# Kernel optimization log

Measured on AMD Instinct MI355X. Metric: run time of the kernel, lower is better.

## Reference

```python
import jax, jax.numpy as jnp
import numpy as np

B, T, IN, H, STEPS = 32768, 11, 2, 64, 80


def gru_cell(x, h, W_ih, W_hh, b_ih, b_hh):
    # PyTorch GRU cell: gates ordered (r, z, n)
    gi = x @ W_ih.T + b_ih            # [B, 3H]
    gh = h @ W_hh.T + b_hh            # [B, 3H]
    gi_r, gi_z, gi_n = jnp.split(gi, 3, axis=-1)
    gh_r, gh_z, gh_n = jnp.split(gh, 3, axis=-1)
    r = jax.nn.sigmoid(gi_r + gh_r)
    z = jax.nn.sigmoid(gi_z + gh_z)
    n = jnp.tanh(gi_n + r * gh_n)
    return (1.0 - z) * n + z * h


def setup_inputs() -> dict:
    key = jax.random.key(0)
    ks = jax.random.split(key, 20)
    s = 1.0 / np.sqrt(H)
    u = lambda k, shape: jax.random.uniform(k, shape, jnp.float32, -s, s)
    inp = {"x": jax.random.normal(ks[0], (B, T, IN), jnp.float32)}
    i = 1
    for pfx, in0 in (("e", IN), ("d", IN)):
        for l, d_in in ((0, in0), (1, H)):
            inp[f"{pfx}W_ih{l}"] = u(ks[i], (3 * H, d_in)); i += 1
            inp[f"{pfx}W_hh{l}"] = u(ks[i], (3 * H, H)); i += 1
            inp[f"{pfx}b_ih{l}"] = u(ks[i], (3 * H,)); i += 1
            inp[f"{pfx}b_hh{l}"] = u(ks[i], (3 * H,)); i += 1
    inp["fc_W"] = u(ks[17], (2, H))
    inp["fc_b"] = u(ks[18], (2,))
    return inp


def reference(x, eW_ih0, eW_hh0, eb_ih0, eb_hh0, eW_ih1, eW_hh1, eb_ih1, eb_hh1,
              dW_ih0, dW_hh0, db_ih0, db_hh0, dW_ih1, dW_hh1, db_ih1, db_hh1,
              fc_W, fc_b):
    b = x.shape[0]
    h0 = jnp.zeros((b, H), x.dtype)
    h1 = jnp.zeros((b, H), x.dtype)

    # ---- encoder: 2-layer GRU over time (dropout inactive in eval) ----
    def enc_step(carry, xt):
        c0, c1 = carry
        c0 = gru_cell(xt, c0, eW_ih0, eW_hh0, eb_ih0, eb_hh0)
        c1 = gru_cell(c0, c1, eW_ih1, eW_hh1, eb_ih1, eb_hh1)
        return (c0, c1), None

    (h0, h1), _ = jax.lax.scan(enc_step, (h0, h1), jnp.swapaxes(x, 0, 1))

    def dec_step(carry, _):
        inp, c0, c1 = carry
        c0 = gru_cell(inp, c0, dW_ih0, dW_hh0, db_ih0, db_hh0)
        c1 = gru_cell(c0, c1, dW_ih1, dW_hh1, db_ih1, db_hh1)
        pred = c1 @ fc_W.T + fc_b     # [B, 2]
        return (pred, c0, c1), pred

    init = (x[:, -1, :], h0, h1)
    _, preds = jax.lax.scan(dec_step, init, None, length=STEPS)  # [80, B, 2]
    return jnp.swapaxes(preds, 0, 1)  # [B, 80, 2]
```

## Files before the change

### kernel.cpp

```cpp
#include <hip/hip_runtime.h>
#include <cstddef>

#define T_SEQ 11
#define STEPS 80

typedef _Float16 f16;
typedef _Float16 f16x4 __attribute__((ext_vector_type(4)));
typedef _Float16 f16x8 __attribute__((ext_vector_type(8)));
typedef float    f32x4 __attribute__((ext_vector_type(4)));

#define SRC (-1.44269504f)
#define SNC ( 2.88539008f)

__device__ __forceinline__ f32x4 mfma16(f16x8 a, f16x8 b, f32x4 c) {
    return __builtin_amdgcn_mfma_f32_16x16x32_f16(a, b, c, 0, 0, 0);
}
__device__ __forceinline__ float exp2r(float x) { return __builtin_amdgcn_exp2f(x); }

__device__ __forceinline__ f16x8 wfrag(const float* __restrict__ W, int row, int k0, float sc) {
    f16x8 r;
    #pragma unroll
    for (int i = 0; i < 8; ++i) r[i] = (f16)(sc * W[row * 64 + k0 + i]);
    return r;
}
__device__ __forceinline__ f16x8 cfrag(const float* __restrict__ Wih0,
                                       const float* __restrict__ fcW, int row, int k0, float sc) {
    f16x8 r;
    #pragma unroll
    for (int i = 0; i < 8; ++i)
        r[i] = (f16)(sc * (Wih0[row * 2] * fcW[k0 + i] + Wih0[row * 2 + 1] * fcW[64 + k0 + i]));
    return r;
}

struct WSet {
    f16x8 xR[2], xZ[2], xN[2];
    f16x8 hR[2], hZ[2], hN[2];
    f32x4 bR, bZ, bNi, bNh;
};

__device__ __forceinline__ void load_h_side(WSet& W,
    const float* __restrict__ Whh, const float* __restrict__ bih,
    const float* __restrict__ bhh, int jA, int j4, int quad)
{
    #pragma unroll
    for (int ks = 0; ks < 2; ++ks) {
        const int k0 = ks * 32 + quad * 8;
        W.hR[ks] = wfrag(Whh, jA,       k0, SRC);
        W.hZ[ks] = wfrag(Whh, jA + 64,  k0, SRC);
        W.hN[ks] = wfrag(Whh, jA + 128, k0, SNC);
    }
    #pragma unroll
    for (int rg = 0; rg < 4; ++rg) {
        W.bR[rg]  = SRC * (bih[j4 + rg] + bhh[j4 + rg]);
        W.bZ[rg]  = SRC * (bih[64 + j4 + rg] + bhh[64 + j4 + rg]);
        W.bNi[rg] = SNC * bih[128 + j4 + rg];
        W.bNh[rg] = SNC * bhh[128 + j4 + rg];
    }
}
__device__ __forceinline__ void load_x_side(WSet& W, const float* __restrict__ Wx,
                                            int jA, int quad)
{
    #pragma unroll
    for (int ks = 0; ks < 2; ++ks) {
        const int k0 = ks * 32 + quad * 8;
        W.xR[ks] = wfrag(Wx, jA,       k0, SRC);
        W.xZ[ks] = wfrag(Wx, jA + 64,  k0, SRC);
        W.xN[ks] = wfrag(Wx, jA + 128, k0, SNC);
    }
}

template<bool XM>
__device__ __forceinline__ void cell(const WSet& W,
    const f16* __restrict__ Xs, const f16* __restrict__ Hs, f16* __restrict__ Dst,
    f16x4 (&ho)[4],
    const f32x4* __restrict__ xw, const float2* __restrict__ xv,
    int ro0, int ro1, int wo)
{
    #pragma unroll
    for (int mt = 0; mt < 4; ++mt) {
        const int mo = mt * 1024;
        f16x8 hb0 = *(const f16x8*)(Hs + ro0 + mo);
        f16x8 hb1 = *(const f16x8*)(Hs + ro1 + mo);
        f32x4 aR  = mfma16(W.hR[0], hb0, W.bR);
        f32x4 aZ  = mfma16(W.hZ[0], hb0, W.bZ);
        f32x4 aNh = mfma16(W.hN[0], hb0, W.bNh);
        aR  = mfma16(W.hR[1], hb1, aR);
        aZ  = mfma16(W.hZ[1], hb1, aZ);
        aNh = mfma16(W.hN[1], hb1, aNh);
        f32x4 aNi;
        if constexpr (XM) {
            f16x8 xb0 = *(const f16x8*)(Xs + ro0 + mo);
            f16x8 xb1 = *(const f16x8*)(Xs + ro1 + mo);
            aR  = mfma16(W.xR[0], xb0, aR);    aR  = mfma16(W.xR[1], xb1, aR);
            aZ  = mfma16(W.xZ[0], xb0, aZ);    aZ  = mfma16(W.xZ[1], xb1, aZ);
            aNi = mfma16(W.xN[0], xb0, W.bNi); aNi = mfma16(W.xN[1], xb1, aNi);
        } else {
            const float x0 = xv[mt].x, x1 = xv[mt].y;
            aR  += x0 * xw[0] + x1 * xw[1];
            aZ  += x0 * xw[2] + x1 * xw[3];
            aNi  = W.bNi + x0 * xw[4] + x1 * xw[5];
        }
        f16x4 o;
        #pragma unroll
        for (int i = 0; i < 4; ++i) {
            const float r = __builtin_amdgcn_rcpf(1.f + exp2r(aR[i]));
            const float z = __builtin_amdgcn_rcpf(1.f + exp2r(aZ[i]));
            const float n = 1.f - 2.f * __builtin_amdgcn_rcpf(1.f + exp2r(aNi[i] + r * aNh[i]));
            const float h = n + z * ((float)ho[mt][i] - n);
            o[i] = (f16)h;
        }
        ho[mt] = o;
        *(f16x4*)(Dst + wo + mo) = o;
    }
}

__global__ __launch_bounds__(256, 2)
void gru_traj_mfma8(
    const float* __restrict__ x,
    const float* __restrict__ eWih0, const float* __restrict__ eWhh0,
    const float* __restrict__ ebih0, const float* __restrict__ ebhh0,
    const float* __restrict__ eWih1, const float* __restrict__ eWhh1,
    const float* __restrict__ ebih1, const float* __restrict__ ebhh1,
    const float* __restrict__ dWih0, const float* __restrict__ dWhh0,
    const float* __restrict__ dbih0, const float* __restrict__ dbhh0,
    const float* __restrict__ dWih1, const float* __restrict__ dWhh1,
    const float* __restrict__ dbih1, const float* __restrict__ dbhh1,
    const float* __restrict__ fcW,  const float* __restrict__ fcb,
    float* __restrict__ out)
{
    __shared__ f16 hbuf[4][64 * 64];
    __shared__ float2 xe[T_SEQ * 64];

    const int tid  = threadIdx.x;
    const int lane = tid & 63;
    const int w    = __builtin_amdgcn_readfirstlane(tid >> 6);
    const int quad = lane >> 4;
    const int col  = lane & 15;
    const int r0   = blockIdx.x * 64;

    {
        const float2* x2 = (const float2*)x;
        for (int i = tid; i < 64 * T_SEQ; i += 256) {
            const int row = i / T_SEQ, t = i - row * T_SEQ;
            xe[t * 64 + row] = x2[(size_t)r0 * T_SEQ + i];
        }
    }
    for (int i = tid; i < 64 * 64; i += 256) { hbuf[0][i] = (f16)0.f; hbuf[2][i] = (f16)0.f; }

    const int c7  = col & 7;
    const int ro0 = col * 64 + ((quad ^ c7) << 3);
    const int ro1 = col * 64 + (((4 + quad) ^ c7) << 3);
    const int wo  = col * 64 + ((((w << 1) | (quad >> 1)) ^ c7) << 3) + ((quad & 1) << 2);

    const int jA = w * 16 + col;
    const int j4 = w * 16 + quad * 4;

    f16x4 ho0[4], ho1[4];
    #pragma unroll
    for (int mt = 0; mt < 4; ++mt) {
        #pragma unroll
        for (int i = 0; i < 4; ++i) { ho0[mt][i] = (f16)0.f; ho1[mt][i] = (f16)0.f; }
    }

    WSet W0, W1;
    load_h_side(W0, eWhh0, ebih0, ebhh0, jA, j4, quad);
    load_h_side(W1, eWhh1, ebih1, ebhh1, jA, j4, quad);
    load_x_side(W1, eWih1, jA, quad);
    {
        f32x4 xw[6];
        #pragma unroll
        for (int rg = 0; rg < 4; ++rg) {
            xw[0][rg] = SRC * eWih0[(j4 + rg) * 2];        xw[1][rg] = SRC * eWih0[(j4 + rg) * 2 + 1];
            xw[2][rg] = SRC * eWih0[(64 + j4 + rg) * 2];   xw[3][rg] = SRC * eWih0[(64 + j4 + rg) * 2 + 1];
            xw[4][rg] = SNC * eWih0[(128 + j4 + rg) * 2];  xw[5][rg] = SNC * eWih0[(128 + j4 + rg) * 2 + 1];
        }
        __syncthreads();

        #pragma unroll 1
        for (int t = 0; t < T_SEQ - 1; t += 2) {
            float2 xv[4];
            #pragma unroll
            for (int mt = 0; mt < 4; ++mt) xv[mt] = xe[t * 64 + mt * 16 + col];
            cell<false>(W0, hbuf[0], hbuf[0], hbuf[1], ho0, xw, xv, ro0, ro1, wo);
            __syncthreads();
            cell<true >(W1, hbuf[1], hbuf[2], hbuf[3], ho1, nullptr, nullptr, ro0, ro1, wo);
            #pragma unroll
            for (int mt = 0; mt < 4; ++mt) xv[mt] = xe[(t + 1) * 64 + mt * 16 + col];
            cell<false>(W0, hbuf[1], hbuf[1], hbuf[0], ho0, xw, xv, ro0, ro1, wo);
            __syncthreads();
            cell<true >(W1, hbuf[0], hbuf[3], hbuf[2], ho1, nullptr, nullptr, ro0, ro1, wo);
        }
        {
            float2 xv[4];
            #pragma unroll
            for (int mt = 0; mt < 4; ++mt) xv[mt] = xe[10 * 64 + mt * 16 + col];
            cell<false>(W0, hbuf[0], hbuf[0], hbuf[1], ho0, xw, xv, ro0, ro1, wo);
            __syncthreads();
            cell<true >(W1, hbuf[1], hbuf[2], hbuf[3], ho1, nullptr, nullptr, ro0, ro1, wo);
        }
    }

    load_h_side(W0, dWhh0, dbih0, dbhh0, jA, j4, quad);
    #pragma unroll
    for (int ks = 0; ks < 2; ++ks) {
        const int k0 = ks * 32 + quad * 8;
        W0.xR[ks] = cfrag(dWih0, fcW, jA,       k0, SRC);
        W0.xZ[ks] = cfrag(dWih0, fcW, jA + 64,  k0, SRC);
        W0.xN[ks] = cfrag(dWih0, fcW, jA + 128, k0, SNC);
    }
    #pragma unroll
    for (int rg = 0; rg < 4; ++rg) {
        const int j = j4 + rg;
        W0.bR[rg]  += SRC * (dWih0[j * 2] * fcb[0]         + dWih0[j * 2 + 1] * fcb[1]);
        W0.bZ[rg]  += SRC * (dWih0[(64 + j) * 2] * fcb[0]  + dWih0[(64 + j) * 2 + 1] * fcb[1]);
        W0.bNi[rg] += SNC * (dWih0[(128 + j) * 2] * fcb[0] + dWih0[(128 + j) * 2 + 1] * fcb[1]);
    }
    load_h_side(W1, dWhh1, dbih1, dbhh1, jA, j4, quad);
    load_x_side(W1, dWih1, jA, quad);
    f16x8 fcf[2];
    #pragma unroll
    for (int ks = 0; ks < 2; ++ks) {
        #pragma unroll
        for (int i = 0; i < 8; ++i) fcf[ks][i] = (f16)0.f;
        if (col < 2) fcf[ks] = wfrag(fcW, col, ks * 32 + quad * 8, 1.0f);
    }
    f32x4 pb;
    #pragma unroll
    for (int rg = 0; rg < 4; ++rg) pb[rg] = (quad == 0 && rg < 2) ? fcb[rg] : 0.f;

    float* __restrict__ op = out + (size_t)(r0 + w * 16 + col) * (STEPS * 2);

    {
        f32x4 xw[6];
        #pragma unroll
        for (int rg = 0; rg < 4; ++rg) {
            xw[0][rg] = SRC * dWih0[(j4 + rg) * 2];        xw[1][rg] = SRC * dWih0[(j4 + rg) * 2 + 1];
            xw[2][rg] = SRC * dWih0[(64 + j4 + rg) * 2];   xw[3][rg] = SRC * dWih0[(64 + j4 + rg) * 2 + 1];
            xw[4][rg] = SNC * dWih0[(128 + j4 + rg) * 2];  xw[5][rg] = SNC * dWih0[(128 + j4 + rg) * 2 + 1];
        }
        float2 xv0[4];
        #pragma unroll
        for (int mt = 0; mt < 4; ++mt) xv0[mt] = xe[10 * 64 + mt * 16 + col];
        cell<false>(W0, hbuf[1], hbuf[1], hbuf[0], ho0, xw, xv0, ro0, ro1, wo);
        __syncthreads();
        cell<true >(W1, hbuf[0], hbuf[3], hbuf[2], ho1, nullptr, nullptr, ro0, ro1, wo);
        __syncthreads();
        f16x8 hb0 = *(const f16x8*)(hbuf[2] + ro0 + w * 1024);
        f16x8 hb1 = *(const f16x8*)(hbuf[2] + ro1 + w * 1024);
        f32x4 p = mfma16(fcf[0], hb0, pb);
        p = mfma16(fcf[1], hb1, p);
        if (quad == 0) *(float2*)op = make_float2(p[0], p[1]);
        op += 2;
    }

    #pragma unroll 1
    for (int sp = 0; sp < 39; ++sp) {
        cell<true>(W0, hbuf[2], hbuf[0], hbuf[1], ho0, nullptr, nullptr, ro0, ro1, wo);
        __syncthreads();
        cell<true>(W1, hbuf[1], hbuf[2], hbuf[3], ho1, nullptr, nullptr, ro0, ro1, wo);
        __syncthreads();
        {
            f16x8 hb0 = *(const f16x8*)(hbuf[3] + ro0 + w * 1024);
            f16x8 hb1 = *(const f16x8*)(hbuf[3] + ro1 + w * 1024);
            f32x4 p = mfma16(fcf[0], hb0, pb);
            p = mfma16(fcf[1], hb1, p);
            if (quad == 0) *(float2*)op = make_float2(p[0], p[1]);
            op += 2;
        }
        cell<true>(W0, hbuf[3], hbuf[1], hbuf[0], ho0, nullptr, nullptr, ro0, ro1, wo);
        __syncthreads();
        cell<true>(W1, hbuf[0], hbuf[3], hbuf[2], ho1, nullptr, nullptr, ro0, ro1, wo);
        __syncthreads();
        {
            f16x8 hb0 = *(const f16x8*)(hbuf[2] + ro0 + w * 1024);
            f16x8 hb1 = *(const f16x8*)(hbuf[2] + ro1 + w * 1024);
            f32x4 p = mfma16(fcf[0], hb0, pb);
            p = mfma16(fcf[1], hb1, p);
            if (quad == 0) *(float2*)op = make_float2(p[0], p[1]);
            op += 2;
        }
    }
    {
        cell<true>(W0, hbuf[2], hbuf[0], hbuf[1], ho0, nullptr, nullptr, ro0, ro1, wo);
        __syncthreads();
        cell<true>(W1, hbuf[1], hbuf[2], hbuf[3], ho1, nullptr, nullptr, ro0, ro1, wo);
        __syncthreads();
        f16x8 hb0 = *(const f16x8*)(hbuf[3] + ro0 + w * 1024);
        f16x8 hb1 = *(const f16x8*)(hbuf[3] + ro1 + w * 1024);
        f32x4 p = mfma16(fcf[0], hb0, pb);
        p = mfma16(fcf[1], hb1, p);
        if (quad == 0) *(float2*)op = make_float2(p[0], p[1]);
    }
}

extern "C" void kernel_launch(void* const* d_in, const int* in_sizes, int n_in,
                              void* d_out, int out_size, void* d_ws, size_t ws_size,
                              hipStream_t stream) {
    (void)n_in; (void)out_size; (void)d_ws; (void)ws_size;

    const float* x     = (const float*)d_in[0];
    const float* eWih0 = (const float*)d_in[1];
    const float* eWhh0 = (const float*)d_in[2];
    const float* ebih0 = (const float*)d_in[3];
    const float* ebhh0 = (const float*)d_in[4];
    const float* eWih1 = (const float*)d_in[5];
    const float* eWhh1 = (const float*)d_in[6];
    const float* ebih1 = (const float*)d_in[7];
    const float* ebhh1 = (const float*)d_in[8];
    const float* dWih0 = (const float*)d_in[9];
    const float* dWhh0 = (const float*)d_in[10];
    const float* dbih0 = (const float*)d_in[11];
    const float* dbhh0 = (const float*)d_in[12];
    const float* dWih1 = (const float*)d_in[13];
    const float* dWhh1 = (const float*)d_in[14];
    const float* dbih1 = (const float*)d_in[15];
    const float* dbhh1 = (const float*)d_in[16];
    const float* fcW   = (const float*)d_in[17];
    const float* fcb   = (const float*)d_in[18];
    float* out = (float*)d_out;

    const int b = in_sizes[0] / (T_SEQ * 2);
    dim3 grid(b / 64), block(256);
    hipLaunchKernelGGL(gru_traj_mfma8, grid, block, 0, stream,
        x, eWih0, eWhh0, ebih0, ebhh0, eWih1, eWhh1, ebih1, ebhh1,
        dWih0, dWhh0, dbih0, dbhh0, dWih1, dWhh1, dbih1, dbhh1,
        fcW, fcb, out);
}
```

Measured before the change: 450.4 us.

## Halve rows per block to 32 and raise occupancy to four blocks per CU

Each block now processes 32 batch rows instead of 64, which halves the per-thread hidden-state registers, the per-step MFMA tiles and the shared buffers. The grid doubles and launch bounds ask for four resident blocks per CU instead of two. More resident blocks can hide barrier and MFMA latency in the serial recurrence. In exchange, the per-thread weight fragments are duplicated across twice as many blocks, and only two of the four waves now do the output projection.

Result: slower. 1.621 ms (+259.9%).

```diff
diff --git a/kernel.cpp b/kernel.cpp
--- a/kernel.cpp
+++ b/kernel.cpp
@@ -72,12 +72,12 @@
 template<bool XM>
 __device__ __forceinline__ void cell(const WSet& W,
     const f16* __restrict__ Xs, const f16* __restrict__ Hs, f16* __restrict__ Dst,
-    f16x4 (&ho)[4],
+    f16x4 (&ho)[2],
     const f32x4* __restrict__ xw, const float2* __restrict__ xv,
     int ro0, int ro1, int wo)
 {
     #pragma unroll
-    for (int mt = 0; mt < 4; ++mt) {
+    for (int mt = 0; mt < 2; ++mt) {
         const int mo = mt * 1024;
         f16x8 hb0 = *(const f16x8*)(Hs + ro0 + mo);
         f16x8 hb1 = *(const f16x8*)(Hs + ro1 + mo);
@@ -114,8 +114,8 @@
     }
 }
 
-__global__ __launch_bounds__(256, 2)
-void gru_traj_mfma8(
+__global__ __launch_bounds__(256, 4)
+void gru_traj_mfma9(
     const float* __restrict__ x,
     const float* __restrict__ eWih0, const float* __restrict__ eWhh0,
     const float* __restrict__ ebih0, const float* __restrict__ ebhh0,
@@ -128,24 +128,24 @@
     const float* __restrict__ fcW,  const float* __restrict__ fcb,
     float* __restrict__ out)
 {
-    __shared__ f16 hbuf[4][64 * 64];
-    __shared__ float2 xe[T_SEQ * 64];
+    __shared__ f16 hbuf[4][32 * 64];
+    __shared__ float2 xe[T_SEQ * 32];
 
     const int tid  = threadIdx.x;
     const int lane = tid & 63;
     const int w    = __builtin_amdgcn_readfirstlane(tid >> 6);
     const int quad = lane >> 4;
     const int col  = lane & 15;
-    const int r0   = blockIdx.x * 64;
+    const int r0   = blockIdx.x * 32;
 
     {
         const float2* x2 = (const float2*)x;
-        for (int i = tid; i < 64 * T_SEQ; i += 256) {
+        for (int i = tid; i < 32 * T_SEQ; i += 256) {
             const int row = i / T_SEQ, t = i - row * T_SEQ;
-            xe[t * 64 + row] = x2[(size_t)r0 * T_SEQ + i];
-        }
-    }
-    for (int i = tid; i < 64 * 64; i += 256) { hbuf[0][i] = (f16)0.f; hbuf[2][i] = (f16)0.f; }
+            xe[t * 32 + row] = x2[(size_t)r0 * T_SEQ + i];
+        }
+    }
+    for (int i = tid; i < 32 * 64; i += 256) { hbuf[0][i] = (f16)0.f; hbuf[2][i] = (f16)0.f; }
 
     const int c7  = col & 7;
     const int ro0 = col * 64 + ((quad ^ c7) << 3);
@@ -155,9 +155,9 @@
     const int jA = w * 16 + col;
     const int j4 = w * 16 + quad * 4;
 
-    f16x4 ho0[4], ho1[4];
-    #pragma unroll
-    for (int mt = 0; mt < 4; ++mt) {
+    f16x4 ho0[2], ho1[2];
+    #pragma unroll
+    for (int mt = 0; mt < 2; ++mt) {
         #pragma unroll
         for (int i = 0; i < 4; ++i) { ho0[mt][i] = (f16)0.f; ho1[mt][i] = (f16)0.f; }
     }
@@ -178,22 +178,22 @@
 
         #pragma unroll 1
         for (int t = 0; t < T_SEQ - 1; t += 2) {
-            float2 xv[4];
+            float2 xv[2];
             #pragma unroll
-            for (int mt = 0; mt < 4; ++mt) xv[mt] = xe[t * 64 + mt * 16 + col];
+            for (int mt = 0; mt < 2; ++mt) xv[mt] = xe[t * 32 + mt * 16 + col];
             cell<false>(W0, hbuf[0], hbuf[0], hbuf[1], ho0, xw, xv, ro0, ro1, wo);
             __syncthreads();
             cell<true >(W1, hbuf[1], hbuf[2], hbuf[3], ho1, nullptr, nullptr, ro0, ro1, wo);
             #pragma unroll
-            for (int mt = 0; mt < 4; ++mt) xv[mt] = xe[(t + 1) * 64 + mt * 16 + col];
+            for (int mt = 0; mt < 2; ++mt) xv[mt] = xe[(t + 1) * 32 + mt * 16 + col];
             cell<false>(W0, hbuf[1], hbuf[1], hbuf[0], ho0, xw, xv, ro0, ro1, wo);
             __syncthreads();
             cell<true >(W1, hbuf[0], hbuf[3], hbuf[2], ho1, nullptr, nullptr, ro0, ro1, wo);
         }
         {
-            float2 xv[4];
+            float2 xv[2];
             #pragma unroll
-            for (int mt = 0; mt < 4; ++mt) xv[mt] = xe[10 * 64 + mt * 16 + col];
+            for (int mt = 0; mt < 2; ++mt) xv[mt] = xe[10 * 32 + mt * 16 + col];
             cell<false>(W0, hbuf[0], hbuf[0], hbuf[1], ho0, xw, xv, ro0, ro1, wo);
             __syncthreads();
             cell<true >(W1, hbuf[1], hbuf[2], hbuf[3], ho1, nullptr, nullptr, ro0, ro1, wo);
@@ -228,7 +228,8 @@
     #pragma unroll
     for (int rg = 0; rg < 4; ++rg) pb[rg] = (quad == 0 && rg < 2) ? fcb[rg] : 0.f;
 
-    float* __restrict__ op = out + (size_t)(r0 + w * 16 + col) * (STEPS * 2);
+    const int cw = w & 1;
+    float* __restrict__ op = out + (size_t)(r0 + cw * 16 + col) * (STEPS * 2);
 
     {
         f32x4 xw[6];
@@ -238,18 +239,20 @@
             xw[2][rg] = SRC * dWih0[(64 + j4 + rg) * 2];   xw[3][rg] = SRC * dWih0[(64 + j4 + rg) * 2 + 1];
             xw[4][rg] = SNC * dWih0[(128 + j4 + rg) * 2];  xw[5][rg] = SNC * dWih0[(128 + j4 + rg) * 2 + 1];
         }
-        float2 xv0[4];
-        #pragma unroll
-        for (int mt = 0; mt < 4; ++mt) xv0[mt] = xe[10 * 64 + mt * 16 + col];
+        float2 xv0[2];
+        #pragma unroll
+        for (int mt = 0; mt < 2; ++mt) xv0[mt] = xe[10 * 32 + mt * 16 + col];
         cell<false>(W0, hbuf[1], hbuf[1], hbuf[0], ho0, xw, xv0, ro0, ro1, wo);
         __syncthreads();
         cell<true >(W1, hbuf[0], hbuf[3], hbuf[2], ho1, nullptr, nullptr, ro0, ro1, wo);
         __syncthreads();
-        f16x8 hb0 = *(const f16x8*)(hbuf[2] + ro0 + w * 1024);
-        f16x8 hb1 = *(const f16x8*)(hbuf[2] + ro1 + w * 1024);
-        f32x4 p = mfma16(fcf[0], hb0, pb);
-        p = mfma16(fcf[1], hb1, p);
-        if (quad == 0) *(float2*)op = make_float2(p[0], p[1]);
+        if (w < 2) {
+            f16x8 hb0 = *(const f16x8*)(hbuf[2] + ro0 + cw * 1024);
+            f16x8 hb1 = *(const f16x8*)(hbuf[2] + ro1 + cw * 1024);
+            f32x4 p = mfma16(fcf[0], hb0, pb);
+            p = mfma16(fcf[1], hb1, p);
+            if (quad == 0) *(float2*)op = make_float2(p[0], p[1]);
+        }
         op += 2;
     }
 
@@ -259,37 +262,39 @@
         __syncthreads();
         cell<true>(W1, hbuf[1], hbuf[2], hbuf[3], ho1, nullptr, nullptr, ro0, ro1, wo);
         __syncthreads();
-        {
-            f16x8 hb0 = *(const f16x8*)(hbuf[3] + ro0 + w * 1024);
-            f16x8 hb1 = *(const f16x8*)(hbuf[3] + ro1 + w * 1024);
+        if (w < 2) {
+            f16x8 hb0 = *(const f16x8*)(hbuf[3] + ro0 + cw * 1024);
+            f16x8 hb1 = *(const f16x8*)(hbuf[3] + ro1 + cw * 1024);
             f32x4 p = mfma16(fcf[0], hb0, pb);
             p = mfma16(fcf[1], hb1, p);
             if (quad == 0) *(float2*)op = make_float2(p[0], p[1]);
-            op += 2;
-        }
+        }
+        op += 2;
         cell<true>(W0, hbuf[3], hbuf[1], hbuf[0], ho0, nullptr, nullptr, ro0, ro1, wo);
         __syncthreads();
         cell<true>(W1, hbuf[0], hbuf[3], hbuf[2], ho1, nullptr, nullptr, ro0, ro1, wo);
         __syncthreads();
-        {
-            f16x8 hb0 = *(const f16x8*)(hbuf[2] + ro0 + w * 1024);
-            f16x8 hb1 = *(const f16x8*)(hbuf[2] + ro1 + w * 1024);
+        if (w < 2) {
+            f16x8 hb0 = *(const f16x8*)(hbuf[2] + ro0 + cw * 1024);
+            f16x8 hb1 = *(const f16x8*)(hbuf[2] + ro1 + cw * 1024);
             f32x4 p = mfma16(fcf[0], hb0, pb);
             p = mfma16(fcf[1], hb1, p);
             if (quad == 0) *(float2*)op = make_float2(p[0], p[1]);
-            op += 2;
-        }
+        }
+        op += 2;
     }
     {
         cell<true>(W0, hbuf[2], hbuf[0], hbuf[1], ho0, nullptr, nullptr, ro0, ro1, wo);
         __syncthreads();
         cell<true>(W1, hbuf[1], hbuf[2], hbuf[3], ho1, nullptr, nullptr, ro0, ro1, wo);
         __syncthreads();
-        f16x8 hb0 = *(const f16x8*)(hbuf[3] + ro0 + w * 1024);
-        f16x8 hb1 = *(const f16x8*)(hbuf[3] + ro1 + w * 1024);
-        f32x4 p = mfma16(fcf[0], hb0, pb);
-        p = mfma16(fcf[1], hb1, p);
-        if (quad == 0) *(float2*)op = make_float2(p[0], p[1]);
+        if (w < 2) {
+            f16x8 hb0 = *(const f16x8*)(hbuf[3] + ro0 + cw * 1024);
+            f16x8 hb1 = *(const f16x8*)(hbuf[3] + ro1 + cw * 1024);
+            f32x4 p = mfma16(fcf[0], hb0, pb);
+            p = mfma16(fcf[1], hb1, p);
+            if (quad == 0) *(float2*)op = make_float2(p[0], p[1]);
+        }
     }
 }
 
@@ -320,8 +325,8 @@
     float* out = (float*)d_out;
 
     const int b = in_sizes[0] / (T_SEQ * 2);
-    dim3 grid(b / 64), block(256);
-    hipLaunchKernelGGL(gru_traj_mfma8, grid, block, 0, stream,
+    dim3 grid(b / 32), block(256);
+    hipLaunchKernelGGL(gru_traj_mfma9, grid, block, 0, stream,
         x, eWih0, eWhh0, ebih0, ebhh0, eWih1, eWhh1, ebih1, ebhh1,
         dWih0, dWhh0, dbih0, dbhh0, dWih1, dWhh1, dbih1, dbhh1,
         fcW, fcb, out);
```

## Stage GRU weights in LDS and spread m-tiles across sixteen waves

Applied to the files above, without the earlier changes.

Moves all recurrent and input weight fragments out of per-thread registers into a pre-swizzled fp16 layout in dynamic LDS (about 143 KB). The block grows from 256 to 1024 threads: each of the 16 waves now computes a single 16-row m-tile for one 16-column gate slice, where each wave previously handled four m-tiles sequentially. Biases, input weights and the composed decoder input weights are also precomputed into LDS, with the decoder set restaged after the encoder finishes. The aim is to cut register pressure and expose more waves per step, at the cost of extra LDS reads for weights on every step and only one resident block per CU.

Measured after the change: 535.2 us. 1.19x slower.

```diff
diff --git a/kernel.cpp b/kernel.cpp
--- a/kernel.cpp
+++ b/kernel.cpp
@@ -12,110 +12,100 @@
 #define SRC (-1.44269504f)
 #define SNC ( 2.88539008f)
 
+#define OFF_WF   0
+#define OFF_HB   98304
+#define OFF_XE   131072
+#define OFF_BIAS 136704
+#define OFF_XW   140800
+#define OFF_FCF  143872
+#define SMEM_BYTES 145920
+
 __device__ __forceinline__ f32x4 mfma16(f16x8 a, f16x8 b, f32x4 c) {
     return __builtin_amdgcn_mfma_f32_16x16x32_f16(a, b, c, 0, 0, 0);
 }
 __device__ __forceinline__ float exp2r(float x) { return __builtin_amdgcn_exp2f(x); }
 
-__device__ __forceinline__ f16x8 wfrag(const float* __restrict__ W, int row, int k0, float sc) {
-    f16x8 r;
+__device__ __forceinline__ void stage_mat(f16* __restrict__ sw, int slot,
+                                          const float* __restrict__ W, int tid) {
+    for (int e = tid; e < 12288; e += 1024) {
+        const int row = e >> 6, k = e & 63;
+        const int g = row >> 6, j = row & 63;
+        const int lane = ((k >> 3) & 3) * 16 + (j & 15);
+        const float sc = (g == 2) ? SNC : SRC;
+        sw[slot * 12288 + g * 4096 + (j >> 4) * 1024 + (k >> 5) * 512 + lane * 8 + (k & 7)]
+            = (f16)(sc * W[e]);
+    }
+}
+__device__ __forceinline__ void stage_composed(f16* __restrict__ sw, int slot,
+                                               const float* __restrict__ Wih0,
+                                               const float* __restrict__ fcW, int tid) {
+    for (int e = tid; e < 12288; e += 1024) {
+        const int row = e >> 6, k = e & 63;
+        const int g = row >> 6, j = row & 63;
+        const int lane = ((k >> 3) & 3) * 16 + (j & 15);
+        const float sc = (g == 2) ? SNC : SRC;
+        const float v = Wih0[row * 2] * fcW[k] + Wih0[row * 2 + 1] * fcW[64 + k];
+        sw[slot * 12288 + g * 4096 + (j >> 4) * 1024 + (k >> 5) * 512 + lane * 8 + (k & 7)]
+            = (f16)(sc * v);
+    }
+}
+
+template<bool XM, int SH, int SX, int CT>
+__device__ __forceinline__ void cellL(
+    const f16* __restrict__ sw, const float* __restrict__ sb, const float* __restrict__ sxw,
+    const f16* __restrict__ Xs, const f16* __restrict__ Hs, f16* __restrict__ Dst,
+    f16x4& ho, int wb, int j4, int rom0, int rom1, int wom, float x0, float x1)
+{
+    const f16* whb = sw + SH * 12288 + wb;
+    const f32x4 bR  = *(const f32x4*)(sb + CT * 256 +       j4);
+    const f32x4 bZ  = *(const f32x4*)(sb + CT * 256 +  64 + j4);
+    const f32x4 bNi = *(const f32x4*)(sb + CT * 256 + 128 + j4);
+    const f32x4 bNh = *(const f32x4*)(sb + CT * 256 + 192 + j4);
+    f16x8 hb0 = *(const f16x8*)(Hs + rom0);
+    f16x8 hb1 = *(const f16x8*)(Hs + rom1);
+    f32x4 aR  = mfma16(*(const f16x8*)(whb),        hb0, bR);
+    f32x4 aZ  = mfma16(*(const f16x8*)(whb + 4096), hb0, bZ);
+    f32x4 aNh = mfma16(*(const f16x8*)(whb + 8192), hb0, bNh);
+    aR  = mfma16(*(const f16x8*)(whb +  512),       hb1, aR);
+    aZ  = mfma16(*(const f16x8*)(whb + 4096 + 512), hb1, aZ);
+    aNh = mfma16(*(const f16x8*)(whb + 8192 + 512), hb1, aNh);
+    f32x4 aNi;
+    if constexpr (XM) {
+        const f16* wxb = sw + SX * 12288 + wb;
+        f16x8 xb0 = *(const f16x8*)(Xs + rom0);
+        f16x8 xb1 = *(const f16x8*)(Xs + rom1);
+        aR  = mfma16(*(const f16x8*)(wxb),               xb0, aR);
+        aR  = mfma16(*(const f16x8*)(wxb +  512),        xb1, aR);
+        aZ  = mfma16(*(const f16x8*)(wxb + 4096),        xb0, aZ);
+        aZ  = mfma16(*(const f16x8*)(wxb + 4096 + 512),  xb1, aZ);
+        aNi = mfma16(*(const f16x8*)(wxb + 8192),        xb0, bNi);
+        aNi = mfma16(*(const f16x8*)(wxb + 8192 + 512),  xb1, aNi);
+    } else {
+        const f32x4 xw0 = *(const f32x4*)(sxw +        j4);
+        const f32x4 xw1 = *(const f32x4*)(sxw +  64 + j4);
+        const f32x4 xw2 = *(const f32x4*)(sxw + 128 + j4);
+        const f32x4 xw3 = *(const f32x4*)(sxw + 192 + j4);
+        const f32x4 xw4 = *(const f32x4*)(sxw + 256 + j4);
+        const f32x4 xw5 = *(const f32x4*)(sxw + 320 + j4);
+        aR  += x0 * xw0 + x1 * xw1;
+        aZ  += x0 * xw2 + x1 * xw3;
+        aNi  = bNi + x0 * xw4 + x1 * xw5;
+    }
+    f16x4 o;
     #pragma unroll
-    for (int i = 0; i < 8; ++i) r[i] = (f16)(sc * W[row * 64 + k0 + i]);
-    return r;
-}
-__device__ __forceinline__ f16x8 cfrag(const float* __restrict__ Wih0,
-                                       const float* __restrict__ fcW, int row, int k0, float sc) {
-    f16x8 r;
-    #pragma unroll
-    for (int i = 0; i < 8; ++i)
-        r[i] = (f16)(sc * (Wih0[row * 2] * fcW[k0 + i] + Wih0[row * 2 + 1] * fcW[64 + k0 + i]));
-    return r;
-}
-
-struct WSet {
-    f16x8 xR[2], xZ[2], xN[2];
-    f16x8 hR[2], hZ[2], hN[2];
-    f32x4 bR, bZ, bNi, bNh;
-};
-
-__device__ __forceinline__ void load_h_side(WSet& W,
-    const float* __restrict__ Whh, const float* __restrict__ bih,
-    const float* __restrict__ bhh, int jA, int j4, int quad)
-{
-    #pragma unroll
-    for (int ks = 0; ks < 2; ++ks) {
-        const int k0 = ks * 32 + quad * 8;
-        W.hR[ks] = wfrag(Whh, jA,       k0, SRC);
-        W.hZ[ks] = wfrag(Whh, jA + 64,  k0, SRC);
-        W.hN[ks] = wfrag(Whh, jA + 128, k0, SNC);
-    }
-    #pragma unroll
-    for (int rg = 0; rg < 4; ++rg) {
-        W.bR[rg]  = SRC * (bih[j4 + rg] + bhh[j4 + rg]);
-        W.bZ[rg]  = SRC * (bih[64 + j4 + rg] + bhh[64 + j4 + rg]);
-        W.bNi[rg] = SNC * bih[128 + j4 + rg];
-        W.bNh[rg] = SNC * bhh[128 + j4 + rg];
-    }
-}
-__device__ __forceinline__ void load_x_side(WSet& W, const float* __restrict__ Wx,
-                                            int jA, int quad)
-{
-    #pragma unroll
-    for (int ks = 0; ks < 2; ++ks) {
-        const int k0 = ks * 32 + quad * 8;
-        W.xR[ks] = wfrag(Wx, jA,       k0, SRC);
-        W.xZ[ks] = wfrag(Wx, jA + 64,  k0, SRC);
-        W.xN[ks] = wfrag(Wx, jA + 128, k0, SNC);
-    }
-}
-
-template<bool XM>
-__device__ __forceinline__ void cell(const WSet& W,
-    const f16* __restrict__ Xs, const f16* __restrict__ Hs, f16* __restrict__ Dst,
-    f16x4 (&ho)[4],
-    const f32x4* __restrict__ xw, const float2* __restrict__ xv,
-    int ro0, int ro1, int wo)
-{
-    #pragma unroll
-    for (int mt = 0; mt < 4; ++mt) {
-        const int mo = mt * 1024;
-        f16x8 hb0 = *(const f16x8*)(Hs + ro0 + mo);
-        f16x8 hb1 = *(const f16x8*)(Hs + ro1 + mo);
-        f32x4 aR  = mfma16(W.hR[0], hb0, W.bR);
-        f32x4 aZ  = mfma16(W.hZ[0], hb0, W.bZ);
-        f32x4 aNh = mfma16(W.hN[0], hb0, W.bNh);
-        aR  = mfma16(W.hR[1], hb1, aR);
-        aZ  = mfma16(W.hZ[1], hb1, aZ);
-        aNh = mfma16(W.hN[1], hb1, aNh);
-        f32x4 aNi;
-        if constexpr (XM) {
-            f16x8 xb0 = *(const f16x8*)(Xs + ro0 + mo);
-            f16x8 xb1 = *(const f16x8*)(Xs + ro1 + mo);
-            aR  = mfma16(W.xR[0], xb0, aR);    aR  = mfma16(W.xR[1], xb1, aR);
-            aZ  = mfma16(W.xZ[0], xb0, aZ);    aZ  = mfma16(W.xZ[1], xb1, aZ);
-            aNi = mfma16(W.xN[0], xb0, W.bNi); aNi = mfma16(W.xN[1], xb1, aNi);
-        } else {
-            const float x0 = xv[mt].x, x1 = xv[mt].y;
-            aR  += x0 * xw[0] + x1 * xw[1];
-            aZ  += x0 * xw[2] + x1 * xw[3];
-            aNi  = W.bNi + x0 * xw[4] + x1 * xw[5];
-        }
-        f16x4 o;
-        #pragma unroll
-        for (int i = 0; i < 4; ++i) {
-            const float r = __builtin_amdgcn_rcpf(1.f + exp2r(aR[i]));
-            const float z = __builtin_amdgcn_rcpf(1.f + exp2r(aZ[i]));
-            const float n = 1.f - 2.f * __builtin_amdgcn_rcpf(1.f + exp2r(aNi[i] + r * aNh[i]));
-            const float h = n + z * ((float)ho[mt][i] - n);
-            o[i] = (f16)h;
-        }
-        ho[mt] = o;
-        *(f16x4*)(Dst + wo + mo) = o;
-    }
-}
-
-__global__ __launch_bounds__(256, 2)
-void gru_traj_mfma8(
+    for (int i = 0; i < 4; ++i) {
+        const float r = __builtin_amdgcn_rcpf(1.f + exp2r(aR[i]));
+        const float z = __builtin_amdgcn_rcpf(1.f + exp2r(aZ[i]));
+        const float n = 1.f - 2.f * __builtin_amdgcn_rcpf(1.f + exp2r(aNi[i] + r * aNh[i]));
+        const float h = n + z * ((float)ho[i] - n);
+        o[i] = (f16)h;
+    }
+    ho = o;
+    *(f16x4*)(Dst + wom) = o;
+}
+
+__global__ __launch_bounds__(1024, 4)
+void gru_traj_lds1(
     const float* __restrict__ x,
     const float* __restrict__ eWih0, const float* __restrict__ eWhh0,
     const float* __restrict__ ebih0, const float* __restrict__ ebhh0,
@@ -128,169 +118,166 @@
     const float* __restrict__ fcW,  const float* __restrict__ fcb,
     float* __restrict__ out)
 {
-    __shared__ f16 hbuf[4][64 * 64];
-    __shared__ float2 xe[T_SEQ * 64];
+    extern __shared__ char smem[];
+    f16*    sw  = (f16*)(smem + OFF_WF);
+    f16*    hbb = (f16*)(smem + OFF_HB);
+    float2* sxe = (float2*)(smem + OFF_XE);
+    float*  sb  = (float*)(smem + OFF_BIAS);
+    float*  sxw = (float*)(smem + OFF_XW);
+    f16*    sfc = (f16*)(smem + OFF_FCF);
+#define HB(i) (hbb + (i) * 4096)
 
     const int tid  = threadIdx.x;
     const int lane = tid & 63;
-    const int w    = __builtin_amdgcn_readfirstlane(tid >> 6);
+    const int wv   = __builtin_amdgcn_readfirstlane(tid >> 6);
+    const int jg   = wv >> 2;
+    const int mg   = wv & 3;
     const int quad = lane >> 4;
     const int col  = lane & 15;
     const int r0   = blockIdx.x * 64;
 
+    stage_mat(sw, 0, eWhh0, tid);
+    stage_mat(sw, 1, eWhh1, tid);
+    stage_mat(sw, 2, eWih1, tid);
     {
         const float2* x2 = (const float2*)x;
-        for (int i = tid; i < 64 * T_SEQ; i += 256) {
+        for (int i = tid; i < 64 * T_SEQ; i += 1024) {
             const int row = i / T_SEQ, t = i - row * T_SEQ;
-            xe[t * 64 + row] = x2[(size_t)r0 * T_SEQ + i];
+            sxe[t * 64 + row] = x2[(size_t)r0 * T_SEQ + i];
         }
     }
-    for (int i = tid; i < 64 * 64; i += 256) { hbuf[0][i] = (f16)0.f; hbuf[2][i] = (f16)0.f; }
-
-    const int c7  = col & 7;
-    const int ro0 = col * 64 + ((quad ^ c7) << 3);
-    const int ro1 = col * 64 + (((4 + quad) ^ c7) << 3);
-    const int wo  = col * 64 + ((((w << 1) | (quad >> 1)) ^ c7) << 3) + ((quad & 1) << 2);
-
-    const int jA = w * 16 + col;
-    const int j4 = w * 16 + quad * 4;
-
-    f16x4 ho0[4], ho1[4];
+    for (int i = tid; i < 4096; i += 1024) { hbb[i] = (f16)0.f; hbb[8192 + i] = (f16)0.f; }
+    if (tid < 64) {
+        const int j = tid;
+        sb[       j] = SRC * (ebih0[j] + ebhh0[j]);
+        sb[ 64 + j] = SRC * (ebih0[64 + j] + ebhh0[64 + j]);
+        sb[128 + j] = SNC * ebih0[128 + j];
+        sb[192 + j] = SNC * ebhh0[128 + j];
+        sb[256 +       j] = SRC * (ebih1[j] + ebhh1[j]);
+        sb[256 +  64 + j] = SRC * (ebih1[64 + j] + ebhh1[64 + j]);
+        sb[256 + 128 + j] = SNC * ebih1[128 + j];
+        sb[256 + 192 + j] = SNC * ebhh1[128 + j];
+        sxw[      j] = SRC * eWih0[j * 2];
+        sxw[ 64 + j] = SRC * eWih0[j * 2 + 1];
+        sxw[128 + j] = SRC * eWih0[(64 + j) * 2];
+        sxw[192 + j] = SRC * eWih0[(64 + j) * 2 + 1];
+        sxw[256 + j] = SNC * eWih0[(128 + j) * 2];
+        sxw[320 + j] = SNC * eWih0[(128 + j) * 2 + 1];
+    }
+    {
+        const int e = tid;
+        const int ks = e >> 9, rr = e & 511;
+        const int lne = rr >> 3, ki = rr & 7;
+        const int c = lne & 15, q = lne >> 4;
+        const int k = ks * 32 + q * 8 + ki;
+        sfc[ks * 512 + lne * 8 + ki] = (c < 2) ? (f16)fcW[c * 64 + k] : (f16)0.f;
+    }
+    __syncthreads();
+
+    const int c7   = col & 7;
+    const int rom0 = col * 64 + ((quad ^ c7) << 3) + mg * 1024;
+    const int rom1 = col * 64 + (((4 + quad) ^ c7) << 3) + mg * 1024;
+    const int wom  = col * 64 + ((((jg << 1) | (quad >> 1)) ^ c7) << 3) + ((quad & 1) << 2) + mg * 1024;
+    const int j4   = jg * 16 + quad * 4;
+    const int wb   = lane * 8 + jg * 1024;
+
+    f16x4 ho0, ho1;
     #pragma unroll
-    for (int mt = 0; mt < 4; ++mt) {
+    for (int i = 0; i < 4; ++i) { ho0[i] = (f16)0.f; ho1[i] = (f16)0.f; }
+
+    #pragma unroll 1
+    for (int t = 0; t < T_SEQ - 1; t += 2) {
+        float2 xv = sxe[t * 64 + mg * 16 + col];
+        cellL<false, 0, 0, 0>(sw, sb, sxw, HB(0), HB(0), HB(1), ho0, wb, j4, rom0, rom1, wom, xv.x, xv.y);
+        __syncthreads();
+        cellL<true, 1, 2, 1>(sw, sb, sxw, HB(1), HB(2), HB(3), ho1, wb, j4, rom0, rom1, wom, 0.f, 0.f);
+        xv = sxe[(t + 1) * 64 + mg * 16 + col];
+        cellL<false, 0, 0, 0>(sw, sb, sxw, HB(1), HB(1), HB(0), ho0, wb, j4, rom0, rom1, wom, xv.x, xv.y);
+        __syncthreads();
+        cellL<true, 1, 2, 1>(sw, sb, sxw, HB(0), HB(3), HB(2), ho1, wb, j4, rom0, rom1, wom, 0.f, 0.f);
+    }
+    {
+        const float2 xv = sxe[10 * 64 + mg * 16 + col];
+        cellL<false, 0, 0, 0>(sw, sb, sxw, HB(0), HB(0), HB(1), ho0, wb, j4, rom0, rom1, wom, xv.x, xv.y);
+        __syncthreads();
+        cellL<true, 1, 2, 1>(sw, sb, sxw, HB(1), HB(2), HB(3), ho1, wb, j4, rom0, rom1, wom, 0.f, 0.f);
+    }
+
+    __syncthreads();
+    stage_mat(sw, 0, dWhh0, tid);
+    stage_mat(sw, 1, dWhh1, tid);
+    stage_mat(sw, 2, dWih1, tid);
+    stage_composed(sw, 3, dWih0, fcW, tid);
+    if (tid < 64) {
+        const int j = tid;
+        const float f0 = fcb[0], f1 = fcb[1];
+        sb[512 +       j] = SRC * (dbih0[j] + dbhh0[j] + dWih0[j * 2] * f0 + dWih0[j * 2 + 1] * f1);
+        sb[512 +  64 + j] = SRC * (dbih0[64 + j] + dbhh0[64 + j] + dWih0[(64 + j) * 2] * f0 + dWih0[(64 + j) * 2 + 1] * f1);
+        sb[512 + 128 + j] = SNC * (dbih0[128 + j] + dWih0[(128 + j) * 2] * f0 + dWih0[(128 + j) * 2 + 1] * f1);
+        sb[512 + 192 + j] = SNC * dbhh0[128 + j];
+        sb[768 +       j] = SRC * (dbih1[j] + dbhh1[j]);
+        sb[768 +  64 + j] = SRC * (dbih1[64 + j] + dbhh1[64 + j]);
+        sb[768 + 128 + j] = SNC * dbih1[128 + j];
+        sb[768 + 192 + j] = SNC * dbhh1[128 + j];
+        sxw[384 +       j] = SRC * dWih0[j * 2];
+        sxw[384 +  64 + j] = SRC * dWih0[j * 2 + 1];
+        sxw[384 + 128 + j] = SRC * dWih0[(64 + j) * 2];
+        sxw[384 + 192 + j] = SRC * dWih0[(64 + j) * 2 + 1];
+        sxw[384 + 256 + j] = SNC * dWih0[(128 + j) * 2];
+        sxw[384 + 320 + j] = SNC * dWih0[(128 + j) * 2 + 1];
+    }
+    __syncthreads();
+
+    f32x4 pb;
+    {
+        const float f0 = fcb[0], f1 = fcb[1];
         #pragma unroll
-        for (int i = 0; i < 4; ++i) { ho0[mt][i] = (f16)0.f; ho1[mt][i] = (f16)0.f; }
-    }
-
-    WSet W0, W1;
-    load_h_side(W0, eWhh0, ebih0, ebhh0, jA, j4, quad);
-    load_h_side(W1, eWhh1, ebih1, ebhh1, jA, j4, quad);
-    load_x_side(W1, eWih1, jA, quad);
-    {
-        f32x4 xw[6];
-        #pragma unroll
-        for (int rg = 0; rg < 4; ++rg) {
-            xw[0][rg] = SRC * eWih0[(j4 + rg) * 2];        xw[1][rg] = SRC * eWih0[(j4 + rg) * 2 + 1];
-            xw[2][rg] = SRC * eWih0[(64 + j4 + rg) * 2];   xw[3][rg] = SRC * eWih0[(64 + j4 + rg) * 2 + 1];
-            xw[4][rg] = SNC * eWih0[(128 + j4 + rg) * 2];  xw[5][rg] = SNC * eWih0[(128 + j4 + rg) * 2 + 1];
+        for (int rg = 0; rg < 4; ++rg) pb[rg] = 0.f;
+        if (quad == 0) { pb[0] = f0; pb[1] = f1; }
+    }
+    float* op = out + (size_t)(r0 + mg * 16 + col) * (STEPS * 2);
+
+    auto FCout = [&](const f16* h1c) {
+        if (jg == 0) {
+            f16x8 a0 = *(const f16x8*)(h1c + rom0);
+            f16x8 a1 = *(const f16x8*)(h1c + rom1);
+            f32x4 p = mfma16(*(const f16x8*)(sfc + lane * 8), a0, pb);
+            p = mfma16(*(const f16x8*)(sfc + 512 + lane * 8), a1, p);
+            if (quad == 0) *(float2*)op = make_float2(p[0], p[1]);
         }
-        __syncthreads();
-
-        #pragma unroll 1
-        for (int t = 0; t < T_SEQ - 1; t += 2) {
-            float2 xv[4];
-            #pragma unroll
-            for (int mt = 0; mt < 4; ++mt) xv[mt] = xe[t * 64 + mt * 16 + col];
-            cell<false>(W0, hbuf[0], hbuf[0], hbuf[1], ho0, xw, xv, ro0, ro1, wo);
-            __syncthreads();
-            cell<true >(W1, hbuf[1], hbuf[2], hbuf[3], ho1, nullptr, nullptr, ro0, ro1, wo);
-            #pragma unroll
-            for (int mt = 0; mt < 4; ++mt) xv[mt] = xe[(t + 1) * 64 + mt * 16 + col];
-            cell<false>(W0, hbuf[1], hbuf[1], hbuf[0], ho0, xw, xv, ro0, ro1, wo);
-            __syncthreads();
-            cell<true >(W1, hbuf[0], hbuf[3], hbuf[2], ho1, nullptr, nullptr, ro0, ro1, wo);
-        }
-        {
-            float2 xv[4];
-            #pragma unroll
-            for (int mt = 0; mt < 4; ++mt) xv[mt] = xe[10 * 64 + mt * 16 + col];
-            cell<false>(W0, hbuf[0], hbuf[0], hbuf[1], ho0, xw, xv, ro0, ro1, wo);
-            __syncthreads();
-            cell<true >(W1, hbuf[1], hbuf[2], hbuf[3], ho1, nullptr, nullptr, ro0, ro1, wo);
-        }
-    }
-
-    load_h_side(W0, dWhh0, dbih0, dbhh0, jA, j4, quad);
-    #pragma unroll
-    for (int ks = 0; ks < 2; ++ks) {
-        const int k0 = ks * 32 + quad * 8;
-        W0.xR[ks] = cfrag(dWih0, fcW, jA,       k0, SRC);
-        W0.xZ[ks] = cfrag(dWih0, fcW, jA + 64,  k0, SRC);
-        W0.xN[ks] = cfrag(dWih0, fcW, jA + 128, k0, SNC);
-    }
-    #pragma unroll
-    for (int rg = 0; rg < 4; ++rg) {
-        const int j = j4 + rg;
-        W0.bR[rg]  += SRC * (dWih0[j * 2] * fcb[0]         + dWih0[j * 2 + 1] * fcb[1]);
-        W0.bZ[rg]  += SRC * (dWih0[(64 + j) * 2] * fcb[0]  + dWih0[(64 + j) * 2 + 1] * fcb[1]);
-        W0.bNi[rg] += SNC * (dWih0[(128 + j) * 2] * fcb[0] + dWih0[(128 + j) * 2 + 1] * fcb[1]);
-    }
-    load_h_side(W1, dWhh1, dbih1, dbhh1, jA, j4, quad);
-    load_x_side(W1, dWih1, jA, quad);
-    f16x8 fcf[2];
-    #pragma unroll
-    for (int ks = 0; ks < 2; ++ks) {
-        #pragma unroll
-        for (int i = 0; i < 8; ++i) fcf[ks][i] = (f16)0.f;
-        if (col < 2) fcf[ks] = wfrag(fcW, col, ks * 32 + quad * 8, 1.0f);
-    }
-    f32x4 pb;
-    #pragma unroll
-    for (int rg = 0; rg < 4; ++rg) pb[rg] = (quad == 0 && rg < 2) ? fcb[rg] : 0.f;
-
-    float* __restrict__ op = out + (size_t)(r0 + w * 16 + col) * (STEPS * 2);
-
-    {
-        f32x4 xw[6];
-        #pragma unroll
-        for (int rg = 0; rg < 4; ++rg) {
-            xw[0][rg] = SRC * dWih0[(j4 + rg) * 2];        xw[1][rg] = SRC * dWih0[(j4 + rg) * 2 + 1];
-            xw[2][rg] = SRC * dWih0[(64 + j4 + rg) * 2];   xw[3][rg] = SRC * dWih0[(64 + j4 + rg) * 2 + 1];
-            xw[4][rg] = SNC * dWih0[(128 + j4 + rg) * 2];  xw[5][rg] = SNC * dWih0[(128 + j4 + rg) * 2 + 1];
-        }
-        float2 xv0[4];
-        #pragma unroll
-        for (int mt = 0; mt < 4; ++mt) xv0[mt] = xe[10 * 64 + mt * 16 + col];
-        cell<false>(W0, hbuf[1], hbuf[1], hbuf[0], ho0, xw, xv0, ro0, ro1, wo);
-        __syncthreads();
-        cell<true >(W1, hbuf[0], hbuf[3], hbuf[2], ho1, nullptr, nullptr, ro0, ro1, wo);
-        __syncthreads();
-        f16x8 hb0 = *(const f16x8*)(hbuf[2] + ro0 + w * 1024);
-        f16x8 hb1 = *(const f16x8*)(hbuf[2] + ro1 + w * 1024);
-        f32x4 p = mfma16(fcf[0], hb0, pb);
-        p = mfma16(fcf[1], hb1, p);
-        if (quad == 0) *(float2*)op = make_float2(p[0], p[1]);
         op += 2;
+    };
+
+    {
+        const float2 xv0 = sxe[10 * 64 + mg * 16 + col];
+        cellL<false, 0, 0, 2>(sw, sb, sxw + 384, HB(1), HB(1), HB(0), ho0, wb, j4, rom0, rom1, wom, xv0.x, xv0.y);
+        __syncthreads();
+        cellL<true, 1, 2, 3>(sw, sb, sxw, HB(0), HB(3), HB(2), ho1, wb, j4, rom0, rom1, wom, 0.f, 0.f);
+        __syncthreads();
+        FCout(HB(2));
     }
 
     #pragma unroll 1
     for (int sp = 0; sp < 39; ++sp) {
-        cell<true>(W0, hbuf[2], hbuf[0], hbuf[1], ho0, nullptr, nullptr, ro0, ro1, wo);
-        __syncthreads();
-        cell<true>(W1, hbuf[1], hbuf[2], hbuf[3], ho1, nullptr, nullptr, ro0, ro1, wo);
-        __syncthreads();
-        {
-            f16x8 hb0 = *(const f16x8*)(hbuf[3] + ro0 + w * 1024);
-            f16x8 hb1 = *(const f16x8*)(hbuf[3] + ro1 + w * 1024);
-            f32x4 p = mfma16(fcf[0], hb0, pb);
-            p = mfma16(fcf[1], hb1, p);
-            if (quad == 0) *(float2*)op = make_float2(p[0], p[1]);
-            op += 2;
-        }
-        cell<true>(W0, hbuf[3], hbuf[1], hbuf[0], ho0, nullptr, nullptr, ro0, ro1, wo);
-        __syncthreads();
-        cell<true>(W1, hbuf[0], hbuf[3], hbuf[2], ho1, nullptr, nullptr, ro0, ro1, wo);
-        __syncthreads();
-        {
-            f16x8 hb0 = *(const f16x8*)(hbuf[2] + ro0 + w * 1024);
-            f16x8 hb1 = *(const f16x8*)(hbuf[2] + ro1 + w * 1024);
-            f32x4 p = mfma16(fcf[0], hb0, pb);
-            p = mfma16(fcf[1], hb1, p);
-            if (quad == 0) *(float2*)op = make_float2(p[0], p[1]);
-            op += 2;
-        }
-    }
-    {
-        cell<true>(W0, hbuf[2], hbuf[0], hbuf[1], ho0, nullptr, nullptr, ro0, ro1, wo);
-        __syncthreads();
-        cell<true>(W1, hbuf[1], hbuf[2], hbuf[3], ho1, nullptr, nullptr, ro0, ro1, wo);
-        __syncthreads();
-        f16x8 hb0 = *(const f16x8*)(hbuf[3] + ro0 + w * 1024);
-        f16x8 hb1 = *(const f16x8*)(hbuf[3] + ro1 + w * 1024);
-        f32x4 p = mfma16(fcf[0], hb0, pb);
-        p = mfma16(fcf[1], hb1, p);
-        if (quad == 0) *(float2*)op = make_float2(p[0], p[1]);
-    }
+        cellL<true, 0, 3, 2>(sw, sb, sxw, HB(2), HB(0), HB(1), ho0, wb, j4, rom0, rom1, wom, 0.f, 0.f);
+        __syncthreads();
+        cellL<true, 1, 2, 3>(sw, sb, sxw, HB(1), HB(2), HB(3), ho1, wb, j4, rom0, rom1, wom, 0.f, 0.f);
+        __syncthreads();
+        FCout(HB(3));
+        cellL<true, 0, 3, 2>(sw, sb, sxw, HB(3), HB(1), HB(0), ho0, wb, j4, rom0, rom1, wom, 0.f, 0.f);
+        __syncthreads();
+        cellL<true, 1, 2, 3>(sw, sb, sxw, HB(0), HB(3), HB(2), ho1, wb, j4, rom0, rom1, wom, 0.f, 0.f);
+        __syncthreads();
+        FCout(HB(2));
+    }
+    {
+        cellL<true, 0, 3, 2>(sw, sb, sxw, HB(2), HB(0), HB(1), ho0, wb, j4, rom0, rom1, wom, 0.f, 0.f);
+        __syncthreads();
+        cellL<true, 1, 2, 3>(sw, sb, sxw, HB(1), HB(2), HB(3), ho1, wb, j4, rom0, rom1, wom, 0.f, 0.f);
+        __syncthreads();
+        FCout(HB(3));
+    }
+#undef HB
 }
 
 extern "C" void kernel_launch(void* const* d_in, const int* in_sizes, int n_in,
@@ -319,9 +306,16 @@
     const float* fcb   = (const float*)d_in[18];
     float* out = (float*)d_out;
 
+    static bool attr_done = false;
+    if (!attr_done) {
+        (void)hipFuncSetAttribute((const void*)gru_traj_lds1,
+                                  hipFuncAttributeMaxDynamicSharedMemorySize, SMEM_BYTES);
+        attr_done = true;
+    }
+
     const int b = in_sizes[0] / (T_SEQ * 2);
-    dim3 grid(b / 64), block(256);
-    hipLaunchKernelGGL(gru_traj_mfma8, grid, block, 0, stream,
+    dim3 grid(b / 64), block(1024);
+    hipLaunchKernelGGL(gru_traj_lds1, grid, block, SMEM_BYTES, stream,
         x, eWih0, eWhh0, ebih0, ebhh0, eWih1, eWhh1, ebih1, ebhh1,
         dWih0, dWhh0, dbih0, dbhh0, dWih1, dWhh1, dbih1, dbhh1,
         fcW, fcb, out);
```
